# Performance work log

Measured on AMD Instinct MI355X. Metric: run time of the kernel, lower is better.

Reference implementation:

```python
import jax, jax.numpy as jnp
import numpy as np

TEXT_DIM = 1024
FEAT_DIM = 1024
NUM_HEADS = 16
HEAD_DIM = FEAT_DIM // NUM_HEADS
EPS = 1e-6


def rms_norm(x, w):
    # LlamaRMSNorm: compute in fp32, scale by learned weight
    xf = x.astype(jnp.float32)
    var = jnp.mean(xf * xf, axis=-1, keepdims=True)
    return (xf * jax.lax.rsqrt(var + EPS)).astype(x.dtype) * w


def setup_inputs() -> dict:
    key = jax.random.key(0)
    ks = jax.random.split(key, 8)
    def xavier(k, shape, gain=1.0):
        fan_in, fan_out = shape[1], shape[0]
        lim = gain * np.sqrt(6.0 / (fan_in + fan_out))
        return jax.random.uniform(k, shape, jnp.float32, -lim, lim)
    return {
        "text": jax.random.normal(ks[0], (8, 512, TEXT_DIM), jnp.float32),
        "features": jax.random.normal(ks[1], (8, 1024, FEAT_DIM), jnp.float32),
        "W_q": xavier(ks[2], (FEAT_DIM, TEXT_DIM)),
        "b_q": jnp.zeros((FEAT_DIM,), jnp.float32),
        "W_k": xavier(ks[3], (FEAT_DIM, FEAT_DIM)),
        "b_k": jnp.zeros((FEAT_DIM,), jnp.float32),
        "W_o": xavier(ks[4], (FEAT_DIM, FEAT_DIM), gain=0.1),
        "b_o": jnp.zeros((FEAT_DIM,), jnp.float32),
        "g_feat": jnp.ones((FEAT_DIM,), jnp.float32),
        "g_q": jnp.ones((FEAT_DIM,), jnp.float32),
        "g_k": jnp.ones((FEAT_DIM,), jnp.float32),
    }


def reference(text, features, W_q, b_q, W_k, b_k, W_o, b_o, g_feat, g_q, g_k):
    B, T, _ = text.shape
    _, N, _ = features.shape
    feats = rms_norm(features, g_feat)                      # [B,N,Df]
    Q = rms_norm(text @ W_q.T + b_q, g_q)                   # [B,T,Df]
    K = rms_norm(feats @ W_k.T + b_k, g_k)                  # [B,N,Df]
    Qh = Q.reshape(B, T, NUM_HEADS, HEAD_DIM)
    Kh = K.reshape(B, N, NUM_HEADS, HEAD_DIM)
    Vh = feats.reshape(B, N, NUM_HEADS, HEAD_DIM)
    scores = jnp.einsum("bthd,bnhd->bhtn", Qh, Kh) / np.sqrt(HEAD_DIM).astype(np.float32)
    attn = jax.nn.softmax(scores, axis=-1)                  # [B,H,T,N]
    out = jnp.einsum("bhtn,bnhd->bthd", attn, Vh).reshape(B, T, FEAT_DIM)
    return out @ W_o.T + b_o
```

## Files before the change

### kernel.cpp

```cpp
#include <hip/hip_runtime.h>
#include <hip/hip_bf16.h>


typedef unsigned short u16;
typedef __bf16 bf16x8 __attribute__((ext_vector_type(8)));
typedef float f32x4 __attribute__((ext_vector_type(4)));

__device__ inline f32x4 mfma16(bf16x8 a, bf16x8 b, f32x4 c) {
    return __builtin_amdgcn_mfma_f32_16x16x32_bf16(a, b, c, 0, 0, 0);
}

__device__ inline u16 f2bf(float f) {
    union { float f; unsigned u; } v; v.f = f;
    unsigned r = v.u + 0x7fffu + ((v.u >> 16) & 1u);
    return (u16)(r >> 16);
}

__device__ inline float bf2f(u16 x) {
    union { unsigned u; float f; } v; v.u = ((unsigned)x) << 16; return v.f;
}

__device__ inline unsigned pk_bf16(float a, float b) {
    union { float f; unsigned u; } x, y; x.f = a; y.f = b;
    return __builtin_amdgcn_perm(y.u + 0x8000u, x.u + 0x8000u, 0x07060302u);
}

__device__ inline void load_lds16(const void* g, void* l) {
    __builtin_amdgcn_global_load_lds(
        (const __attribute__((address_space(1))) void*)g,
        (__attribute__((address_space(3))) void*)l, 16, 0, 0);
}

__global__ __launch_bounds__(256) void cast4_kernel(const float* __restrict__ text,
                                                    const float* __restrict__ Wq,
                                                    const float* __restrict__ Wk,
                                                    const float* __restrict__ Wo,
                                                    u16* __restrict__ otext, u16* __restrict__ oWq,
                                                    u16* __restrict__ oWk, u16* __restrict__ oWo) {
    int i = blockIdx.x * 256 + threadIdx.x;
    const float* src; u16* dst; int off;
    if (i < 1048576)      { src = text; dst = otext; off = i; }
    else if (i < 1310720) { src = Wq;   dst = oWq;   off = i - 1048576; }
    else if (i < 1572864) { src = Wk;   dst = oWk;   off = i - 1310720; }
    else                  { src = Wo;   dst = oWo;   off = i - 1572864; }
    float4 v = ((const float4*)src)[off];
    uint2 p; p.x = pk_bf16(v.x, v.y); p.y = pk_bf16(v.z, v.w);
    ((uint2*)dst)[off] = p;
}

__global__ __launch_bounds__(256) void rmsnorm_kernel(const float* __restrict__ in,
                                                      const float* __restrict__ g,
                                                      u16* __restrict__ out, float scale) {
    int row = blockIdx.x, tid = threadIdx.x;
    float4 v = ((const float4*)(in + (size_t)row * 1024))[tid];
    float ss = v.x * v.x + v.y * v.y + v.z * v.z + v.w * v.w;
    #pragma unroll
    for (int m = 1; m < 64; m <<= 1) ss += __shfl_xor(ss, m, 64);
    __shared__ float ws[4];
    if ((tid & 63) == 0) ws[tid >> 6] = ss;
    __syncthreads();
    float rs = rsqrtf((ws[0] + ws[1] + ws[2] + ws[3]) * (1.0f / 1024.0f) + 1e-6f) * scale;
    float4 gv = ((const float4*)g)[tid];
    uint2 p;
    p.x = pk_bf16(v.x * rs * gv.x, v.y * rs * gv.y);
    p.y = pk_bf16(v.z * rs * gv.z, v.w * rs * gv.w);
    ((uint2*)(out + (size_t)row * 1024))[tid] = p;
}

__global__ __launch_bounds__(256) void rmsnorm_qk_kernel(u16* __restrict__ QK,
                                                         const float* __restrict__ g_q,
                                                         const float* __restrict__ g_k,
                                                         float qscale) {
    int row = blockIdx.x, tid = threadIdx.x;
    const float* g = (row < 4096) ? g_q : g_k;
    float outsc = (row < 4096) ? qscale : 1.0f;
    uint2* rp = (uint2*)(QK + (size_t)row * 1024) + tid;
    union { u16 s[4]; uint2 v; } in; in.v = *rp;
    float x0 = bf2f(in.s[0]), x1 = bf2f(in.s[1]), x2 = bf2f(in.s[2]), x3 = bf2f(in.s[3]);
    float ss = x0 * x0 + x1 * x1 + x2 * x2 + x3 * x3;
    #pragma unroll
    for (int m = 1; m < 64; m <<= 1) ss += __shfl_xor(ss, m, 64);
    __shared__ float ws[4];
    if ((tid & 63) == 0) ws[tid >> 6] = ss;
    __syncthreads();
    float rs = rsqrtf((ws[0] + ws[1] + ws[2] + ws[3]) * (1.0f / 1024.0f) + 1e-6f) * outsc;
    float4 gv = ((const float4*)g)[tid];
    uint2 p;
    p.x = pk_bf16(x0 * rs * gv.x, x1 * rs * gv.y);
    p.y = pk_bf16(x2 * rs * gv.z, x3 * rs * gv.w);
    *rp = p;
}

__global__ __launch_bounds__(256) void transpose_kernel(const u16* __restrict__ in,
                                                        u16* __restrict__ out) {
    __shared__ __align__(16) u16 tile[64][72];
    int tid = threadIdx.x, b = blockIdx.z;
    int n0 = blockIdx.x * 64, d0 = blockIdx.y * 64;
    int r = tid >> 2, cs = (tid & 3) * 16;
    const u16* src = in + ((size_t)(b * 1024 + n0 + r)) * 1024 + d0 + cs;
    union { u16 s[8]; uint4 v; } a0, a1;
    a0.v = *(const uint4*)src;
    a1.v = *(const uint4*)(src + 8);
    #pragma unroll
    for (int i = 0; i < 8; ++i) { tile[r][cs + i] = a0.s[i]; tile[r][cs + 8 + i] = a1.s[i]; }
    __syncthreads();
    union { u16 s[8]; uint4 v; } b0, b1;
    #pragma unroll
    for (int i = 0; i < 8; ++i) { b0.s[i] = tile[cs + i][r]; b1.s[i] = tile[cs + 8 + i][r]; }
    u16* dst = out + ((size_t)(b * 1024 + d0 + r)) * 1024 + n0 + cs;
    *(uint4*)dst = b0.v;
    *(uint4*)(dst + 8) = b1.v;
}

template <bool BF16OUT>
__device__ __forceinline__ void gemm64_tile(const u16* __restrict__ A, const u16* __restrict__ B,
                                            const float* __restrict__ bias, void* __restrict__ Cout,
                                            int m_blk, int n_blk, int K, int N,
                                            u16* As, u16* Bs) {
    int tid = threadIdx.x, wave = tid >> 6, lane = tid & 63;
    int quad = lane >> 4, l15 = lane & 15;
    int wm = wave & 1, wn = wave >> 1;

    f32x4 acc[4][2] = {};

    for (int k0 = 0; k0 < K; k0 += 32) {
        #pragma unroll
        for (int j = 0; j < 2; ++j) {
            int idx = j * 256 + tid;
            int row = idx >> 2, kc = (idx & 3) * 8;
            load_lds16(A + (size_t)(m_blk + row) * K + k0 + kc, As + (j * 256 + wave * 64) * 8);
        }
        {
            int row = tid >> 2, kc = (tid & 3) * 8;
            load_lds16(B + (size_t)(n_blk + row) * K + k0 + kc, Bs + (wave * 64) * 8);
        }
        __syncthreads();
        bf16x8 af[4], bfr[2];
        #pragma unroll
        for (int t = 0; t < 4; ++t)
            af[t] = *(const bf16x8*)&As[(wm * 64 + t * 16 + l15) * 32 + quad * 8];
        #pragma unroll
        for (int t = 0; t < 2; ++t)
            bfr[t] = *(const bf16x8*)&Bs[(wn * 32 + t * 16 + l15) * 32 + quad * 8];
        #pragma unroll
        for (int mt = 0; mt < 4; ++mt)
            #pragma unroll
            for (int nt = 0; nt < 2; ++nt)
                acc[mt][nt] = mfma16(af[mt], bfr[nt], acc[mt][nt]);
        __syncthreads();
    }
    #pragma unroll
    for (int nt = 0; nt < 2; ++nt) {
        int col = n_blk + wn * 32 + nt * 16 + l15;
        float bv = bias[col];
        #pragma unroll
        for (int mt = 0; mt < 4; ++mt) {
            int row0 = m_blk + wm * 64 + mt * 16 + quad * 4;
            #pragma unroll
            for (int r = 0; r < 4; ++r) {
                float val = acc[mt][nt][r] + bv;
                if (BF16OUT) ((u16*)Cout)[(size_t)(row0 + r) * N + col] = f2bf(val);
                else       ((float*)Cout)[(size_t)(row0 + r) * N + col] = val;
            }
        }
    }
}

__global__ __launch_bounds__(256) void gemm_qk_kernel(const u16* __restrict__ text_bf,
                                                      const u16* __restrict__ Wq,
                                                      const u16* __restrict__ feats_bf,
                                                      const u16* __restrict__ Wk,
                                                      const float* __restrict__ b_q,
                                                      const float* __restrict__ b_k,
                                                      u16* __restrict__ QK) {
    __shared__ __align__(16) u16 As[128 * 32];
    __shared__ __align__(16) u16 Bs[64 * 32];
    int id = blockIdx.x;
    if (id < 512) {
        gemm64_tile<true>(text_bf, Wq, b_q, QK, (id & 31) * 128, (id >> 5) * 64, 1024, 1024, As, Bs);
    } else {
        id -= 512;
        gemm64_tile<true>(feats_bf, Wk, b_k, QK + 4096 * 1024,
                          (id & 63) * 128, (id >> 6) * 64, 1024, 1024, As, Bs);
    }
}

__global__ __launch_bounds__(256) void gemm_o_kernel(const u16* __restrict__ A,
                                                     const u16* __restrict__ B,
                                                     const float* __restrict__ bias,
                                                     float* __restrict__ C) {
    __shared__ __align__(16) u16 As[128 * 32];
    __shared__ __align__(16) u16 Bs[64 * 32];
    int id = blockIdx.x;
    gemm64_tile<false>(A, B, bias, C, (id & 31) * 128, (id >> 5) * 64, 1024, 1024, As, Bs);
}

__global__ __launch_bounds__(256) void attn_kernel(const u16* __restrict__ Q,
                                                   const u16* __restrict__ K,
                                                   const u16* __restrict__ Vt,
                                                   u16* __restrict__ Out) {
    int bh = blockIdx.x, qt = blockIdx.y;
    int b = bh >> 4, h = bh & 15;
    int tid = threadIdx.x, wave = tid >> 6, lane = tid & 63;
    int quad = lane >> 4, l15 = lane & 15;

    __shared__ __align__(16) u16 Ks[64 * 64];
    __shared__ __align__(16) u16 Vs[64 * 64];
    __shared__ __align__(16) u16 Plds[4][16 * 72];
    u16* Pw = &Plds[wave][0];

    const size_t qoff = ((size_t)(b * 512 + qt * 64 + wave * 16 + l15)) * 1024 + h * 64 + quad * 8;
    bf16x8 qf0 = *(const bf16x8*)(Q + qoff);
    bf16x8 qf1 = *(const bf16x8*)(Q + qoff + 32);

    int srl = lane >> 3, scl = lane & 7;
    const u16* Kbase = K + ((size_t)(b * 1024)) * 1024 + h * 64;
    const u16* Vbase = Vt + ((size_t)(b * 1024 + h * 64)) * 1024;

    __bf16 onev = (__bf16)1.0f;
    bf16x8 ones = {onev, onev, onev, onev, onev, onev, onev, onev};

    f32x4 o[4] = {};
    f32x4 lac = {0.0f, 0.0f, 0.0f, 0.0f};

    for (int n0 = 0; n0 < 1024; n0 += 64) {
        #pragma unroll
        for (int j = 0; j < 2; ++j) {
            int row = wave * 16 + j * 8 + srl;
            load_lds16(Kbase + (size_t)(n0 + row) * 1024 + (scl ^ srl) * 8,
                       Ks + (wave * 16 + j * 8) * 64);
            load_lds16(Vbase + (size_t)row * 1024 + n0 + (scl ^ srl) * 8,
                       Vs + (wave * 16 + j * 8) * 64);
        }
        __syncthreads();

        f32x4 s[4];
        #pragma unroll
        for (int nt = 0; nt < 4; ++nt) {
            int R = nt * 16 + l15;
            int c1 = (quad ^ (l15 & 7)) * 8;
            bf16x8 kf0 = *(const bf16x8*)&Ks[R * 64 + c1];
            bf16x8 kf1 = *(const bf16x8*)&Ks[R * 64 + (c1 ^ 32)];
            f32x4 z = {-16.0f, -16.0f, -16.0f, -16.0f};
            s[nt] = mfma16(kf0, qf0, z);
            s[nt] = mfma16(kf1, qf1, s[nt]);
        }

        #pragma unroll
        for (int nt = 0; nt < 4; ++nt) {
            uint2 pk;
            pk.x = pk_bf16(exp2f(s[nt][0]), exp2f(s[nt][1]));
            pk.y = pk_bf16(exp2f(s[nt][2]), exp2f(s[nt][3]));
            *(uint2*)&Pw[l15 * 72 + nt * 16 + quad * 4] = pk;
        }

        bf16x8 pf[2];
        #pragma unroll
        for (int kc = 0; kc < 2; ++kc)
            pf[kc] = *(const bf16x8*)&Pw[l15 * 72 + kc * 32 + quad * 8];
        #pragma unroll
        for (int kc = 0; kc < 2; ++kc) {
            lac = mfma16(ones, pf[kc], lac);
            #pragma unroll
            for (int dt = 0; dt < 4; ++dt) {
                int d = dt * 16 + l15;
                int ch = ((kc * 4 + quad) ^ (l15 & 7)) * 8;
                bf16x8 vf = *(const bf16x8*)&Vs[d * 64 + ch];
                o[dt] = mfma16(vf, pf[kc], o[dt]);
            }
        }
        __syncthreads();
    }

    float il = 1.0f / lac[0];
    size_t obase = ((size_t)(b * 512 + qt * 64 + wave * 16 + l15)) * 1024 + h * 64 + quad * 4;
    #pragma unroll
    for (int dt = 0; dt < 4; ++dt) {
        uint2 pk;
        pk.x = pk_bf16(o[dt][0] * il, o[dt][1] * il);
        pk.y = pk_bf16(o[dt][2] * il, o[dt][3] * il);
        *(uint2*)(Out + obase + dt * 16) = pk;
    }
}

extern "C" void kernel_launch(void* const* d_in, const int* in_sizes, int n_in,
                              void* d_out, int out_size, void* d_ws, size_t ws_size,
                              hipStream_t stream) {
    const float* text     = (const float*)d_in[0];
    const float* features = (const float*)d_in[1];
    const float* W_q      = (const float*)d_in[2];
    const float* b_q      = (const float*)d_in[3];
    const float* W_k      = (const float*)d_in[4];
    const float* b_k      = (const float*)d_in[5];
    const float* W_o      = (const float*)d_in[6];
    const float* b_o      = (const float*)d_in[7];
    const float* g_feat   = (const float*)d_in[8];
    const float* g_q      = (const float*)d_in[9];
    const float* g_k      = (const float*)d_in[10];

    char* ws = (char*)d_ws;
    u16* text_bf  = (u16*)(ws + 0);
    u16* Wq_bf    = (u16*)(ws + 8388608);
    u16* Wk_bf    = (u16*)(ws + 10485760);
    u16* Wo_bf    = (u16*)(ws + 12582912);
    u16* feats_bf = (u16*)(ws + 14680064);
    u16* Vt       = (u16*)(ws + 31457280);
    u16* QKbuf    = (u16*)(ws + 48234496);
    u16* attn_bf  = (u16*)(ws + 73400320);

    const float QSCALE = 0.18033688011112042f;

    cast4_kernel<<<7168, 256, 0, stream>>>(text, W_q, W_k, W_o, text_bf, Wq_bf, Wk_bf, Wo_bf);

    rmsnorm_kernel<<<8192, 256, 0, stream>>>(features, g_feat, feats_bf, 1.0f);
    transpose_kernel<<<dim3(16, 16, 8), 256, 0, stream>>>(feats_bf, Vt);

    gemm_qk_kernel<<<1536, 256, 0, stream>>>(text_bf, Wq_bf, feats_bf, Wk_bf, b_q, b_k, QKbuf);
    rmsnorm_qk_kernel<<<12288, 256, 0, stream>>>(QKbuf, g_q, g_k, QSCALE);

    attn_kernel<<<dim3(128, 8), 256, 0, stream>>>(QKbuf, QKbuf + 4096 * 1024, Vt, attn_bf);

    gemm_o_kernel<<<512, 256, 0, stream>>>(attn_bf, Wo_bf, b_o, (float*)d_out);
}
```

Before: 237.7 us.

## Use 128x128 tiles for QK GEMM and XOR-swizzle LDS layout

Adds a 128x128 GEMM tile variant in which each wave computes a 64x64 output block, and uses it for the Q/K projection, halving the grid to 768 blocks and raising data reuse per LDS load. Both GEMM tile paths now apply an XOR swizzle to the k-chunk column when loading global data into LDS and when reading fragments, to reduce LDS bank conflicts. The larger tile doubles the accumulator registers, which may lower occupancy, and the smaller grid may leave some CUs with uneven work.

```diff
diff --git a/kernel.cpp b/kernel.cpp
--- a/kernel.cpp
+++ b/kernel.cpp
@@ -113,6 +113,58 @@
 }
 
 template <bool BF16OUT>
+__device__ __forceinline__ void gemm128_tile(const u16* __restrict__ A, const u16* __restrict__ B,
+                                             const float* __restrict__ bias, void* __restrict__ Cout,
+                                             int m_blk, int n_blk, int K, int N,
+                                             u16* As, u16* Bs) {
+    int tid = threadIdx.x, wave = tid >> 6, lane = tid & 63;
+    int quad = lane >> 4, l15 = lane & 15;
+    int wm = wave & 1, wn = wave >> 1;
+    int sw = (l15 >> 1) & 3;
+
+    f32x4 acc[4][4] = {};
+
+    for (int k0 = 0; k0 < K; k0 += 32) {
+        #pragma unroll
+        for (int j = 0; j < 2; ++j) {
+            int idx = j * 256 + tid;
+            int row = idx >> 2;
+            int c = ((idx & 3) ^ ((idx >> 3) & 3)) * 8;
+            load_lds16(A + (size_t)(m_blk + row) * K + k0 + c, As + (j * 256 + wave * 64) * 8);
+            load_lds16(B + (size_t)(n_blk + row) * K + k0 + c, Bs + (j * 256 + wave * 64) * 8);
+        }
+        __syncthreads();
+        bf16x8 af[4], bfr[4];
+        #pragma unroll
+        for (int t = 0; t < 4; ++t) {
+            af[t]  = *(const bf16x8*)&As[(wm * 64 + t * 16 + l15) * 32 + (quad ^ sw) * 8];
+            bfr[t] = *(const bf16x8*)&Bs[(wn * 64 + t * 16 + l15) * 32 + (quad ^ sw) * 8];
+        }
+        #pragma unroll
+        for (int mt = 0; mt < 4; ++mt)
+            #pragma unroll
+            for (int nt = 0; nt < 4; ++nt)
+                acc[mt][nt] = mfma16(af[mt], bfr[nt], acc[mt][nt]);
+        __syncthreads();
+    }
+    #pragma unroll
+    for (int nt = 0; nt < 4; ++nt) {
+        int col = n_blk + wn * 64 + nt * 16 + l15;
+        float bv = bias[col];
+        #pragma unroll
+        for (int mt = 0; mt < 4; ++mt) {
+            int row0 = m_blk + wm * 64 + mt * 16 + quad * 4;
+            #pragma unroll
+            for (int r = 0; r < 4; ++r) {
+                float val = acc[mt][nt][r] + bv;
+                if (BF16OUT) ((u16*)Cout)[(size_t)(row0 + r) * N + col] = f2bf(val);
+                else       ((float*)Cout)[(size_t)(row0 + r) * N + col] = val;
+            }
+        }
+    }
+}
+
+template <bool BF16OUT>
 __device__ __forceinline__ void gemm64_tile(const u16* __restrict__ A, const u16* __restrict__ B,
                                             const float* __restrict__ bias, void* __restrict__ Cout,
                                             int m_blk, int n_blk, int K, int N,
@@ -120,6 +172,7 @@
     int tid = threadIdx.x, wave = tid >> 6, lane = tid & 63;
     int quad = lane >> 4, l15 = lane & 15;
     int wm = wave & 1, wn = wave >> 1;
+    int sw = (l15 >> 1) & 3;
 
     f32x4 acc[4][2] = {};
 
@@ -127,21 +180,23 @@
         #pragma unroll
         for (int j = 0; j < 2; ++j) {
             int idx = j * 256 + tid;
-            int row = idx >> 2, kc = (idx & 3) * 8;
-            load_lds16(A + (size_t)(m_blk + row) * K + k0 + kc, As + (j * 256 + wave * 64) * 8);
+            int row = idx >> 2;
+            int c = ((idx & 3) ^ ((idx >> 3) & 3)) * 8;
+            load_lds16(A + (size_t)(m_blk + row) * K + k0 + c, As + (j * 256 + wave * 64) * 8);
         }
         {
-            int row = tid >> 2, kc = (tid & 3) * 8;
-            load_lds16(B + (size_t)(n_blk + row) * K + k0 + kc, Bs + (wave * 64) * 8);
+            int row = tid >> 2;
+            int c = ((tid & 3) ^ ((tid >> 3) & 3)) * 8;
+            load_lds16(B + (size_t)(n_blk + row) * K + k0 + c, Bs + (wave * 64) * 8);
         }
         __syncthreads();
         bf16x8 af[4], bfr[2];
         #pragma unroll
         for (int t = 0; t < 4; ++t)
-            af[t] = *(const bf16x8*)&As[(wm * 64 + t * 16 + l15) * 32 + quad * 8];
+            af[t] = *(const bf16x8*)&As[(wm * 64 + t * 16 + l15) * 32 + (quad ^ sw) * 8];
         #pragma unroll
         for (int t = 0; t < 2; ++t)
-            bfr[t] = *(const bf16x8*)&Bs[(wn * 32 + t * 16 + l15) * 32 + quad * 8];
+            bfr[t] = *(const bf16x8*)&Bs[(wn * 32 + t * 16 + l15) * 32 + (quad ^ sw) * 8];
         #pragma unroll
         for (int mt = 0; mt < 4; ++mt)
             #pragma unroll
@@ -174,14 +229,14 @@
                                                       const float* __restrict__ b_k,
                                                       u16* __restrict__ QK) {
     __shared__ __align__(16) u16 As[128 * 32];
-    __shared__ __align__(16) u16 Bs[64 * 32];
+    __shared__ __align__(16) u16 Bs[128 * 32];
     int id = blockIdx.x;
-    if (id < 512) {
-        gemm64_tile<true>(text_bf, Wq, b_q, QK, (id & 31) * 128, (id >> 5) * 64, 1024, 1024, As, Bs);
+    if (id < 256) {
+        gemm128_tile<true>(text_bf, Wq, b_q, QK, (id & 31) * 128, (id >> 5) * 128, 1024, 1024, As, Bs);
     } else {
-        id -= 512;
-        gemm64_tile<true>(feats_bf, Wk, b_k, QK + 4096 * 1024,
-                          (id & 63) * 128, (id >> 6) * 64, 1024, 1024, As, Bs);
+        id -= 256;
+        gemm128_tile<true>(feats_bf, Wk, b_k, QK + 4096 * 1024,
+                           (id & 63) * 128, (id >> 6) * 128, 1024, 1024, As, Bs);
     }
 }
 
@@ -315,7 +370,7 @@
     rmsnorm_kernel<<<8192, 256, 0, stream>>>(features, g_feat, feats_bf, 1.0f);
     transpose_kernel<<<dim3(16, 16, 8), 256, 0, stream>>>(feats_bf, Vt);
 
-    gemm_qk_kernel<<<1536, 256, 0, stream>>>(text_bf, Wq_bf, feats_bf, Wk_bf, b_q, b_k, QKbuf);
+    gemm_qk_kernel<<<768, 256, 0, stream>>>(text_bf, Wq_bf, feats_bf, Wk_bf, b_q, b_k, QKbuf);
     rmsnorm_qk_kernel<<<12288, 256, 0, stream>>>(QKbuf, g_q, g_k, QSCALE);
 
     attn_kernel<<<dim3(128, 8), 256, 0, stream>>>(QKbuf, QKbuf + 4096 * 1024, Vt, attn_bf);
```

After: 240.2 us. No clear change (+1.0%).
